# Optimization experiments

Measured on AMD Instinct MI355X. Metric: run time of the kernel, lower is better.

Reference implementation:

```python
import jax, jax.numpy as jnp
import numpy as np

EPS = 1e-5
NUM_GROUPS = 32


def group_norm(x, scale, bias):
    # x: [B, C, H, W], 32 groups, normalized over (C/G, H, W)
    B, C, H, W = x.shape
    G = NUM_GROUPS
    xg = x.reshape(B, G, C // G, H, W)
    mean = xg.mean(axis=(2, 3, 4), keepdims=True)
    var = xg.var(axis=(2, 3, 4), keepdims=True)
    xg = (xg - mean) * jax.lax.rsqrt(var + EPS)
    x = xg.reshape(B, C, H, W)
    return x * scale[None, :, None, None] + bias[None, :, None, None]


def setup_inputs() -> dict:
    key = jax.random.key(0)
    ks = jax.random.split(key, 6)
    B, C, H, W = 32, 512, 32, 32
    std = 1.0 / np.sqrt(C)
    return {
        "x": jax.random.normal(ks[0], (B, C, H, W), dtype=jnp.float32),
        "gn_scale": jnp.ones((C,), dtype=jnp.float32),
        "gn_bias": jnp.zeros((C,), dtype=jnp.float32),
        "wq": jax.random.normal(ks[1], (C, C), dtype=jnp.float32) * std,
        "bq": jnp.zeros((C,), dtype=jnp.float32),
        "wk": jax.random.normal(ks[2], (C, C), dtype=jnp.float32) * std,
        "bk": jnp.zeros((C,), dtype=jnp.float32),
        "wv": jax.random.normal(ks[3], (C, C), dtype=jnp.float32) * std,
        "bv": jnp.zeros((C,), dtype=jnp.float32),
        "wo": jax.random.normal(ks[4], (C, C), dtype=jnp.float32) * std,
        "bo": jnp.zeros((C,), dtype=jnp.float32),
    }


def reference(x, gn_scale, gn_bias, wq, bq, wk, bk, wv, bv, wo, bo):
    B, C, H, W = x.shape
    h = group_norm(x, gn_scale, gn_bias)
    # 1x1 convs == per-pixel matmuls; flatten spatial to tokens: [B, HW, C]
    ht = h.reshape(B, C, H * W).transpose(0, 2, 1)
    q = jnp.einsum('bnc,oc->bno', ht, wq) + bq  # [B, HW, C]
    k = jnp.einsum('bnc,oc->bno', ht, wk) + bk
    v = jnp.einsum('bnc,oc->bno', ht, wv) + bv
    scale = 1.0 / jnp.sqrt(jnp.asarray(C, x.dtype))
    w = jnp.einsum('bnc,bmc->bnm', q, k) * scale  # [B, HW, HW]
    w = jax.nn.softmax(w, axis=-1)
    a = jnp.einsum('bnm,bmc->bnc', w, v)  # [B, HW, C]
    out = jnp.einsum('bnc,oc->bno', a, wo) + bo
    out = out.transpose(0, 2, 1).reshape(B, C, H, W)
    return x + out
```

## Files before the change

### kernel.cpp

```cpp
#include <hip/hip_runtime.h>
#include <stdint.h>

typedef unsigned short u16;
typedef __attribute__((ext_vector_type(8))) short short8;
typedef __attribute__((ext_vector_type(4))) short s16x4;
typedef __attribute__((ext_vector_type(4))) float f32x4;

#define NTOK 1024
#define CDIM 512
#define NG 32

#define GLOAD_LDS16(gptr, lptr)                                                              \
  __builtin_amdgcn_global_load_lds((const __attribute__((address_space(1))) unsigned int*)(gptr), \
                                   (__attribute__((address_space(3))) unsigned int*)(lptr), 16, 0, 0)

__device__ __forceinline__ u16 f2bf(float f) {
  union { float f; uint32_t u; } v; v.f = f;
  uint32_t r = v.u + 0x7fffu + ((v.u >> 16) & 1u);
  return (u16)(r >> 16);
}

__device__ __forceinline__ float bf2f(u16 b) {
  union { uint32_t u; float f; } v; v.u = ((uint32_t)b) << 16;
  return v.f;
}

__global__ __launch_bounds__(256) void wconv(const float* __restrict__ wq, const float* __restrict__ wk,
                                             const float* __restrict__ wv, const float* __restrict__ wo,
                                             const float* __restrict__ bq, const float* __restrict__ bk,
                                             const float* __restrict__ bv,
                                             u16* __restrict__ out, float* __restrict__ bqkv) {
  int i = blockIdx.x * 256 + threadIdx.x;
  out[i]          = f2bf(wq[i]);
  out[262144 + i] = f2bf(wk[i]);
  out[524288 + i] = f2bf(wv[i]);
  out[786432 + i] = f2bf(wo[i]);
  if (i < 512) bqkv[i] = bq[i];
  else if (i < 1024) bqkv[i] = bk[i - 512];
  else if (i < 1536) bqkv[i] = bv[i - 1024];
}

__global__ __launch_bounds__(256) void gn_stats(const float* __restrict__ x,
                                                float* __restrict__ mean_o, float* __restrict__ rstd_o) {
  int bg = blockIdx.x;
  const float4* base = (const float4*)(x + (size_t)bg * 16384);
  float s = 0.f, ss = 0.f;
  for (int i = threadIdx.x; i < 4096; i += 256) {
    float4 v = base[i];
    s  += v.x + v.y + v.z + v.w;
    ss += v.x * v.x + v.y * v.y + v.z * v.z + v.w * v.w;
  }
#pragma unroll
  for (int d = 1; d < 64; d <<= 1) { s += __shfl_xor(s, d); ss += __shfl_xor(ss, d); }
  __shared__ float as[4], as2[4];
  int w = threadIdx.x >> 6;
  if ((threadIdx.x & 63) == 0) { as[w] = s; as2[w] = ss; }
  __syncthreads();
  if (threadIdx.x == 0) {
    float S = as[0] + as[1] + as[2] + as[3];
    float SS = as2[0] + as2[1] + as2[2] + as2[3];
    float m = S * (1.f / 16384.f);
    float var = SS * (1.f / 16384.f) - m * m;
    mean_o[bg] = m;
    rstd_o[bg] = rsqrtf(var + 1e-5f);
  }
}

__global__ __launch_bounds__(256) void gn_apply(const float* __restrict__ x,
                                                const float* __restrict__ mean_, const float* __restrict__ rstd_,
                                                const float* __restrict__ gsc, const float* __restrict__ gbi,
                                                u16* __restrict__ h) {
  int n0 = blockIdx.x * 64, c0 = blockIdx.y * 64, b = blockIdx.z;
  __shared__ u16 t[64][65];
  int tid = threadIdx.x;
  int nl4 = (tid & 15) * 4;
  int clb = tid >> 4;
#pragma unroll
  for (int p = 0; p < 4; ++p) {
    int cl = p * 16 + clb;
    int c = c0 + cl;
    int g = c >> 4;
    float m = mean_[b * NG + g], rs = rstd_[b * NG + g];
    float sc = gsc[c] * rs, bi = gbi[c] - m * sc;
    float4 v = *(const float4*)(x + ((size_t)b * CDIM + c) * NTOK + n0 + nl4);
    t[cl][nl4 + 0] = f2bf(v.x * sc + bi);
    t[cl][nl4 + 1] = f2bf(v.y * sc + bi);
    t[cl][nl4 + 2] = f2bf(v.z * sc + bi);
    t[cl][nl4 + 3] = f2bf(v.w * sc + bi);
  }
  __syncthreads();
  int nl = tid >> 3;
  int cc = (tid & 7) * 8;
#pragma unroll
  for (int p = 0; p < 2; ++p) {
    int n = nl + p * 32;
    short8 o;
#pragma unroll
    for (int i = 0; i < 8; ++i) o[i] = (short)t[cc + i][n];
    *(short8*)(h + (size_t)(b * NTOK + n0 + n) * CDIM + c0 + cc) = o;
  }
}

template <int MODE>
__device__ __forceinline__ void gemm_body(const u16* __restrict__ A, const u16* __restrict__ B,
                                          const float* __restrict__ bias, u16* __restrict__ outb,
                                          u16* __restrict__ outb2,
                                          float* __restrict__ outf, const float* __restrict__ resid,
                                          int Ka, int Kb, int nkt,
                                          size_t strideA, size_t strideB, int batch0) {
  int nx = gridDim.x, ny = gridDim.y;
  int nwg = nx * ny * gridDim.z;
  int id = blockIdx.x + nx * (blockIdx.y + ny * blockIdx.z);
  int cpx = nwg >> 3;
  int sw = (id & 7) * cpx + (id >> 3);
  int bx = sw % nx; int t_ = sw / nx;
  int by = t_ % ny; int z = t_ / ny;

  const u16* Amat = A + (size_t)z * strideA;
  const u16* Bmat = B + (size_t)z * strideB;
  int n0 = bx * 128, m0 = by * 256;
  __shared__ __align__(16) u16 SH[36864];
  int tid = threadIdx.x;
  int l = tid & 63, wid = tid >> 6;
  int lr = l & 15, lh = l >> 4;
  int wm = (wid >> 1) * 64;
  int wn = (wid & 1) * 64;

  f32x4 acc[4][4];
#pragma unroll
  for (int i = 0; i < 4; ++i)
#pragma unroll
    for (int j = 0; j < 4; ++j) acc[i][j] = (f32x4){0.f, 0.f, 0.f, 0.f};

  short8 af[4];
  short8 bfr[4];

  int sr = tid >> 2, sc4 = tid & 3;
  int sg = (sc4 ^ ((sr >> 1) & 3)) * 8;
  const u16* Ag0 = Amat + (size_t)(m0 + sr) * Ka + sg;
  const u16* Ag1 = Ag0 + (size_t)128 * Ka;
  const u16* Bg0 = Bmat + (size_t)(n0 + sr) * Kb + sg;
  u16* Al0 = SH + sr * 32 + sc4 * 8;
  u16* Bl0 = SH + 24576 + sr * 32 + sc4 * 8;

  int rch = (lh ^ ((lr >> 1) & 3)) * 8;

#define STAGE(bufsel, ktv)                                                \
  {                                                                       \
    GLOAD_LDS16(Ag0 + (ktv) * 32, Al0 + (bufsel) * 8192);                 \
    GLOAD_LDS16(Ag1 + (ktv) * 32, Al0 + (bufsel) * 8192 + 4096);          \
    GLOAD_LDS16(Bg0 + (ktv) * 32, Bl0 + (bufsel) * 4096);                 \
  }

#define READ_FRAGS(bufsel)                                                            \
  _Pragma("unroll") for (int i_ = 0; i_ < 4; ++i_)                                    \
    af[i_] = *(const short8*)(SH + (bufsel) * 8192 + (wm + i_ * 16 + lr) * 32 + rch); \
  _Pragma("unroll") for (int j_ = 0; j_ < 4; ++j_)                                    \
    bfr[j_] = *(const short8*)(SH + 24576 + (bufsel) * 4096 + (wn + j_ * 16 + lr) * 32 + rch);

#define MFMA16()                                                                      \
  _Pragma("unroll") for (int i_ = 0; i_ < 4; ++i_)                                    \
    _Pragma("unroll") for (int j_ = 0; j_ < 4; ++j_)                                  \
      acc[i_][j_] = __builtin_amdgcn_mfma_f32_16x16x32_bf16(af[i_], bfr[j_], acc[i_][j_], 0, 0, 0);

  STAGE(0, 0);
  STAGE(1, 1);
  asm volatile("s_waitcnt vmcnt(3)");
  __builtin_amdgcn_sched_barrier(0);
  __builtin_amdgcn_s_barrier();

  int bc = 0, bs = 2;
  for (int t = 0; t < nkt; ++t) {
    const bool more = (t + 2 < nkt);
    if (more) STAGE(bs, t + 2);
    READ_FRAGS(bc);
    __builtin_amdgcn_s_setprio(1);
    MFMA16();
    __builtin_amdgcn_s_setprio(0);
    if (more) { asm volatile("s_waitcnt vmcnt(3)"); }
    else      { asm volatile("s_waitcnt vmcnt(0)"); }
    __builtin_amdgcn_sched_barrier(0);
    __builtin_amdgcn_s_barrier();
    bc = (bc == 2) ? 0 : bc + 1;
    bs = (bs == 2) ? 0 : bs + 1;
  }

  __syncthreads();
  const int gr0 = m0 + wm, gc0 = n0 + wn;
  u16* eb = SH + wid * 4352;

  if constexpr (MODE == 5) {
    float bj[4];
#pragma unroll
    for (int j = 0; j < 4; ++j) bj[j] = bias[gc0 + j * 16 + lr];
    if (n0 < 1024) {
#pragma unroll
      for (int i2 = 0; i2 < 4; ++i2)
#pragma unroll
        for (int j = 0; j < 4; ++j)
#pragma unroll
          for (int r = 0; r < 4; ++r)
            eb[(i2 * 16 + lh * 4 + r) * 68 + j * 16 + lr] = f2bf(acc[i2][j][r] + bj[j]);
      asm volatile("s_waitcnt lgkmcnt(0)");
      __builtin_amdgcn_sched_barrier(0);
#pragma unroll
      for (int t = 0; t < 8; ++t) {
        int row = t * 8 + (l >> 3), c8 = (l & 7) * 8;
        s16x4 lo = *(const s16x4*)(eb + row * 68 + c8);
        s16x4 hi = *(const s16x4*)(eb + row * 68 + c8 + 4);
        short8 o;
        o[0] = lo[0]; o[1] = lo[1]; o[2] = lo[2]; o[3] = lo[3];
        o[4] = hi[0]; o[5] = hi[1]; o[6] = hi[2]; o[7] = hi[3];
        *(short8*)(outb + (size_t)(gr0 + row) * 1024 + gc0 + c8) = o;
      }
    } else {
      int ch0 = gc0 - 1024;
      int bt = m0 >> 10, tok0 = (m0 & 1023) + wm;
#pragma unroll
      for (int i2 = 0; i2 < 4; ++i2)
#pragma unroll
        for (int j = 0; j < 4; ++j) {
          s16x4 w;
#pragma unroll
          for (int r = 0; r < 4; ++r) w[r] = (short)f2bf(acc[i2][j][r] + bj[j]);
          *(s16x4*)(eb + (j * 16 + lr) * 68 + i2 * 16 + lh * 4) = w;
        }
      asm volatile("s_waitcnt lgkmcnt(0)");
      __builtin_amdgcn_sched_barrier(0);
#pragma unroll
      for (int t = 0; t < 8; ++t) {
        int row = t * 8 + (l >> 3), c8 = (l & 7) * 8;
        s16x4 lo = *(const s16x4*)(eb + row * 68 + c8);
        s16x4 hi = *(const s16x4*)(eb + row * 68 + c8 + 4);
        short8 o;
        o[0] = lo[0]; o[1] = lo[1]; o[2] = lo[2]; o[3] = lo[3];
        o[4] = hi[0]; o[5] = hi[1]; o[6] = hi[2]; o[7] = hi[3];
        *(short8*)(outb2 + (size_t)(bt * 512 + ch0 + row) * 1024 + tok0 + c8) = o;
      }
    }
  } else if constexpr (MODE == 3 || MODE == 4) {
    u16* obase = (MODE == 3) ? (outb + (size_t)z * 1048576)
                             : (outb + (size_t)(batch0 + z) * 524288);
    const int LD = (MODE == 3) ? 1024 : 512;
#pragma unroll
    for (int i2 = 0; i2 < 4; ++i2)
#pragma unroll
      for (int j = 0; j < 4; ++j)
#pragma unroll
        for (int r = 0; r < 4; ++r)
          eb[(i2 * 16 + lh * 4 + r) * 68 + j * 16 + lr] = f2bf(acc[i2][j][r]);
    asm volatile("s_waitcnt lgkmcnt(0)");
    __builtin_amdgcn_sched_barrier(0);
#pragma unroll
    for (int t = 0; t < 8; ++t) {
      int row = t * 8 + (l >> 3), c8 = (l & 7) * 8;
      s16x4 lo = *(const s16x4*)(eb + row * 68 + c8);
      s16x4 hi = *(const s16x4*)(eb + row * 68 + c8 + 4);
      short8 o;
      o[0] = lo[0]; o[1] = lo[1]; o[2] = lo[2]; o[3] = lo[3];
      o[4] = hi[0]; o[5] = hi[1]; o[6] = hi[2]; o[7] = hi[3];
      *(short8*)(obase + (size_t)(gr0 + row) * LD + gc0 + c8) = o;
    }
  } else {
    float* ebf = (float*)SH + wid * 2176;
    int bt = n0 >> 10, nn0 = (n0 & 1023) + wn;
#pragma unroll
    for (int pass = 0; pass < 2; ++pass) {
#pragma unroll
      for (int i2 = 0; i2 < 2; ++i2)
#pragma unroll
        for (int r = 0; r < 4; ++r) {
          float bv = bias[gr0 + pass * 32 + i2 * 16 + lh * 4 + r];
#pragma unroll
          for (int j = 0; j < 4; ++j)
            ebf[(i2 * 16 + lh * 4 + r) * 68 + j * 16 + lr] = acc[pass * 2 + i2][j][r] + bv;
        }
      asm volatile("s_waitcnt lgkmcnt(0)");
      __builtin_amdgcn_sched_barrier(0);
#pragma unroll
      for (int t = 0; t < 8; ++t) {
        int row = t * 4 + (l >> 4), c4 = (l & 15) * 4;
        float4 vv = *(const float4*)(ebf + row * 68 + c4);
        size_t addr = ((size_t)bt * 512 + gr0 + pass * 32 + row) * 1024 + nn0 + c4;
        const float4 rr = *(const float4*)(resid + addr);
        vv.x += rr.x; vv.y += rr.y; vv.z += rr.z; vv.w += rr.w;
        *(float4*)(outf + addr) = vv;
      }
      asm volatile("s_waitcnt lgkmcnt(0)");
      __builtin_amdgcn_sched_barrier(0);
    }
  }
#undef STAGE
#undef READ_FRAGS
#undef MFMA16
}

__global__ __launch_bounds__(512, 4) void gemm_qkv(const u16* A, const u16* B, const float* bias,
                                                   u16* outb, u16* outb2, float* outf, const float* resid,
                                                   int Ka, int Kb, int nkt, size_t sA, size_t sB, int b0) {
  gemm_body<5>(A, B, bias, outb, outb2, outf, resid, Ka, Kb, nkt, sA, sB, b0);
}
__global__ __launch_bounds__(512, 4) void gemm_o(const u16* A, const u16* B, const float* bias,
                                                 u16* outb, u16* outb2, float* outf, const float* resid,
                                                 int Ka, int Kb, int nkt, size_t sA, size_t sB, int b0) {
  gemm_body<2>(A, B, bias, outb, outb2, outf, resid, Ka, Kb, nkt, sA, sB, b0);
}
__global__ __launch_bounds__(512, 4) void gemm_s(const u16* A, const u16* B, const float* bias,
                                                 u16* outb, u16* outb2, float* outf, const float* resid,
                                                 int Ka, int Kb, int nkt, size_t sA, size_t sB, int b0) {
  gemm_body<3>(A, B, bias, outb, outb2, outf, resid, Ka, Kb, nkt, sA, sB, b0);
}
__global__ __launch_bounds__(512, 4) void gemm_pv(const u16* A, const u16* B, const float* bias,
                                                  u16* outb, u16* outb2, float* outf, const float* resid,
                                                  int Ka, int Kb, int nkt, size_t sA, size_t sB, int b0) {
  gemm_body<4>(A, B, bias, outb, outb2, outf, resid, Ka, Kb, nkt, sA, sB, b0);
}

__global__ __launch_bounds__(256) void softmax_rows(u16* __restrict__ S) {
  const float scale = 0.04419417382415922f;
  int row = blockIdx.x * 4 + (threadIdx.x >> 6);
  int l = threadIdx.x & 63;
  u16* Sr = S + (size_t)row * 1024;
  short8 a = *(const short8*)(Sr + l * 8);
  short8 b = *(const short8*)(Sr + 512 + l * 8);
  float f[16];
#pragma unroll
  for (int i = 0; i < 8; ++i) { f[i] = bf2f((u16)a[i]); f[8 + i] = bf2f((u16)b[i]); }
  float mx = f[0];
#pragma unroll
  for (int i = 1; i < 16; ++i) mx = fmaxf(mx, f[i]);
#pragma unroll
  for (int d = 1; d < 64; d <<= 1) mx = fmaxf(mx, __shfl_xor(mx, d));
  float s = 0.f;
#pragma unroll
  for (int i = 0; i < 16; ++i) { f[i] = __expf((f[i] - mx) * scale); s += f[i]; }
#pragma unroll
  for (int d = 1; d < 64; d <<= 1) s += __shfl_xor(s, d);
  float inv = 1.f / s;
  short8 oa, ob;
#pragma unroll
  for (int i = 0; i < 8; ++i) { oa[i] = (short)f2bf(f[i] * inv); ob[i] = (short)f2bf(f[8 + i] * inv); }
  *(short8*)(Sr + l * 8) = oa;
  *(short8*)(Sr + 512 + l * 8) = ob;
}

extern "C" void kernel_launch(void* const* d_in, const int* in_sizes, int n_in,
                              void* d_out, int out_size, void* d_ws, size_t ws_size,
                              hipStream_t stream) {
  const float* x   = (const float*)d_in[0];
  const float* gsc = (const float*)d_in[1];
  const float* gbi = (const float*)d_in[2];
  const float* wq  = (const float*)d_in[3];
  const float* bq  = (const float*)d_in[4];
  const float* wk  = (const float*)d_in[5];
  const float* bk  = (const float*)d_in[6];
  const float* wv  = (const float*)d_in[7];
  const float* bv  = (const float*)d_in[8];
  const float* wo  = (const float*)d_in[9];
  const float* bo  = (const float*)d_in[10];

  char* ws = (char*)d_ws;
  u16* wbf = (u16*)ws;
  float* bqkv = (float*)(ws + (2ull << 20));
  float* mean_ = (float*)(ws + (2ull << 20) + 65536);
  float* rstd_ = mean_ + 1024;
  u16* h   = (u16*)(ws + (4ull << 20));
  u16* qk  = (u16*)(ws + (36ull << 20));
  u16* vm  = (u16*)(ws + (100ull << 20));
  u16* S   = (u16*)(ws + (132ull << 20));
  u16* am  = h;
  float* out = (float*)d_out;

  size_t sbytes = ws_size > (132ull << 20) ? ws_size - (132ull << 20) : 0;
  int CB = 1;
  while (CB < 32 && (size_t)(CB * 2) * (2ull << 20) <= sbytes) CB *= 2;

  wconv<<<1024, 256, 0, stream>>>(wq, wk, wv, wo, bq, bk, bv, wbf, bqkv);
  gn_stats<<<1024, 256, 0, stream>>>(x, mean_, rstd_);
  gn_apply<<<dim3(16, 8, 32), 256, 0, stream>>>(x, mean_, rstd_, gsc, gbi, h);
  gemm_qkv<<<dim3(12, 128), 512, 0, stream>>>(h, wbf, bqkv, qk, vm, nullptr, nullptr,
                                              512, 512, 16, 0, 0, 0);
  for (int c0 = 0; c0 < 32; c0 += CB) {
    gemm_s<<<dim3(8, 4, CB), 512, 0, stream>>>(qk + (size_t)c0 * 1048576, qk + 512 + (size_t)c0 * 1048576,
                                               nullptr, S, nullptr, nullptr, nullptr,
                                               1024, 1024, 16, 1048576, 1048576, 0);
    softmax_rows<<<CB * 256, 256, 0, stream>>>(S);
    gemm_pv<<<dim3(4, 4, CB), 512, 0, stream>>>(S, vm + (size_t)c0 * 524288,
                                                nullptr, am, nullptr, nullptr, nullptr,
                                                1024, 1024, 32, 1048576, 524288, c0);
  }
  gemm_o<<<dim3(256, 2), 512, 0, stream>>>(wbf + 786432, am, bo, nullptr, nullptr, out, x,
                                           512, 512, 16, 0, 0, 0);
}
```

Measured before the change: 248.3 us.

## Halve GEMM workgroup to four waves with 128x64 per-wave tiles

All four GEMM kernels now run 256 threads (4 waves) per 256x128 block instead of 8 waves. Each wave computes a 128x64 output tile with 8x4 MFMA accumulators, and the staging issues six global-to-LDS loads per thread per k-step. Epilogues are split into two passes so the per-wave LDS scratch still fits. The larger per-wave tile raises register reuse of fragments, but accumulator register pressure roughly doubles and occupancy drops (launch bounds 256,2), which can expose memory latency.

Measured after the change: 248.2 us. No clear change (-0.0%).

```diff
diff --git a/kernel.cpp b/kernel.cpp
--- a/kernel.cpp
+++ b/kernel.cpp
@@ -123,49 +123,51 @@
   int tid = threadIdx.x;
   int l = tid & 63, wid = tid >> 6;
   int lr = l & 15, lh = l >> 4;
-  int wm = (wid >> 1) * 64;
+  int wm = (wid >> 1) * 128;
   int wn = (wid & 1) * 64;
 
-  f32x4 acc[4][4];
-#pragma unroll
-  for (int i = 0; i < 4; ++i)
+  f32x4 acc[8][4];
+#pragma unroll
+  for (int i = 0; i < 8; ++i)
 #pragma unroll
     for (int j = 0; j < 4; ++j) acc[i][j] = (f32x4){0.f, 0.f, 0.f, 0.f};
 
-  short8 af[4];
+  short8 af[8];
   short8 bfr[4];
 
   int sr = tid >> 2, sc4 = tid & 3;
   int sg = (sc4 ^ ((sr >> 1) & 3)) * 8;
   const u16* Ag0 = Amat + (size_t)(m0 + sr) * Ka + sg;
-  const u16* Ag1 = Ag0 + (size_t)128 * Ka;
   const u16* Bg0 = Bmat + (size_t)(n0 + sr) * Kb + sg;
   u16* Al0 = SH + sr * 32 + sc4 * 8;
   u16* Bl0 = SH + 24576 + sr * 32 + sc4 * 8;
 
   int rch = (lh ^ ((lr >> 1) & 3)) * 8;
 
-#define STAGE(bufsel, ktv)                                                \
-  {                                                                       \
-    GLOAD_LDS16(Ag0 + (ktv) * 32, Al0 + (bufsel) * 8192);                 \
-    GLOAD_LDS16(Ag1 + (ktv) * 32, Al0 + (bufsel) * 8192 + 4096);          \
-    GLOAD_LDS16(Bg0 + (ktv) * 32, Bl0 + (bufsel) * 4096);                 \
+#define STAGE(bufsel, ktv)                                                        \
+  {                                                                               \
+    GLOAD_LDS16(Ag0 + (ktv) * 32,                       Al0 + (bufsel) * 8192);   \
+    GLOAD_LDS16(Ag0 + (ktv) * 32 + (size_t)64  * Ka,    Al0 + (bufsel) * 8192 + 2048); \
+    GLOAD_LDS16(Ag0 + (ktv) * 32 + (size_t)128 * Ka,    Al0 + (bufsel) * 8192 + 4096); \
+    GLOAD_LDS16(Ag0 + (ktv) * 32 + (size_t)192 * Ka,    Al0 + (bufsel) * 8192 + 6144); \
+    GLOAD_LDS16(Bg0 + (ktv) * 32,                       Bl0 + (bufsel) * 4096);   \
+    GLOAD_LDS16(Bg0 + (ktv) * 32 + (size_t)64  * Kb,    Bl0 + (bufsel) * 4096 + 2048); \
   }
 
 #define READ_FRAGS(bufsel)                                                            \
-  _Pragma("unroll") for (int i_ = 0; i_ < 4; ++i_)                                    \
+  _Pragma("unroll") for (int i_ = 0; i_ < 8; ++i_)                                    \
     af[i_] = *(const short8*)(SH + (bufsel) * 8192 + (wm + i_ * 16 + lr) * 32 + rch); \
   _Pragma("unroll") for (int j_ = 0; j_ < 4; ++j_)                                    \
     bfr[j_] = *(const short8*)(SH + 24576 + (bufsel) * 4096 + (wn + j_ * 16 + lr) * 32 + rch);
 
-#define MFMA16()                                                                      \
-  _Pragma("unroll") for (int i_ = 0; i_ < 4; ++i_)                                    \
+#define MFMA32()                                                                      \
+  _Pragma("unroll") for (int i_ = 0; i_ < 8; ++i_)                                    \
     _Pragma("unroll") for (int j_ = 0; j_ < 4; ++j_)                                  \
       acc[i_][j_] = __builtin_amdgcn_mfma_f32_16x16x32_bf16(af[i_], bfr[j_], acc[i_][j_], 0, 0, 0);
 
   STAGE(0, 0);
   STAGE(1, 1);
-  asm volatile("s_waitcnt vmcnt(3)");
+  asm volatile("s_waitcnt vmcnt(6)");
   __builtin_amdgcn_sched_barrier(0);
   __builtin_amdgcn_s_barrier();
 
@@ -175,9 +177,9 @@
     if (more) STAGE(bs, t + 2);
     READ_FRAGS(bc);
     __builtin_amdgcn_s_setprio(1);
-    MFMA16();
+    MFMA32();
     __builtin_amdgcn_s_setprio(0);
-    if (more) { asm volatile("s_waitcnt vmcnt(3)"); }
+    if (more) { asm volatile("s_waitcnt vmcnt(6)"); }
     else      { asm volatile("s_waitcnt vmcnt(0)"); }
     __builtin_amdgcn_sched_barrier(0);
     __builtin_amdgcn_s_barrier();
@@ -195,12 +197,73 @@
     for (int j = 0; j < 4; ++j) bj[j] = bias[gc0 + j * 16 + lr];
     if (n0 < 1024) {
 #pragma unroll
+      for (int pass = 0; pass < 2; ++pass) {
+#pragma unroll
+        for (int i2 = 0; i2 < 4; ++i2)
+#pragma unroll
+          for (int j = 0; j < 4; ++j)
+#pragma unroll
+            for (int r = 0; r < 4; ++r)
+              eb[(i2 * 16 + lh * 4 + r) * 68 + j * 16 + lr] =
+                  f2bf(acc[pass * 4 + i2][j][r] + bj[j]);
+        asm volatile("s_waitcnt lgkmcnt(0)");
+        __builtin_amdgcn_sched_barrier(0);
+#pragma unroll
+        for (int t = 0; t < 8; ++t) {
+          int row = t * 8 + (l >> 3), c8 = (l & 7) * 8;
+          s16x4 lo = *(const s16x4*)(eb + row * 68 + c8);
+          s16x4 hi = *(const s16x4*)(eb + row * 68 + c8 + 4);
+          short8 o;
+          o[0] = lo[0]; o[1] = lo[1]; o[2] = lo[2]; o[3] = lo[3];
+          o[4] = hi[0]; o[5] = hi[1]; o[6] = hi[2]; o[7] = hi[3];
+          *(short8*)(outb + (size_t)(gr0 + pass * 64 + row) * 1024 + gc0 + c8) = o;
+        }
+        asm volatile("s_waitcnt lgkmcnt(0)");
+        __builtin_amdgcn_sched_barrier(0);
+      }
+    } else {
+      int ch0 = gc0 - 1024;
+      int bt = m0 >> 10, tok0 = (m0 & 1023) + wm;
+#pragma unroll
+      for (int pass = 0; pass < 2; ++pass) {
+#pragma unroll
+        for (int i2 = 0; i2 < 4; ++i2)
+#pragma unroll
+          for (int j = 0; j < 4; ++j) {
+            s16x4 w;
+#pragma unroll
+            for (int r = 0; r < 4; ++r) w[r] = (short)f2bf(acc[pass * 4 + i2][j][r] + bj[j]);
+            *(s16x4*)(eb + (j * 16 + lr) * 68 + i2 * 16 + lh * 4) = w;
+          }
+        asm volatile("s_waitcnt lgkmcnt(0)");
+        __builtin_amdgcn_sched_barrier(0);
+#pragma unroll
+        for (int t = 0; t < 8; ++t) {
+          int row = t * 8 + (l >> 3), c8 = (l & 7) * 8;
+          s16x4 lo = *(const s16x4*)(eb + row * 68 + c8);
+          s16x4 hi = *(const s16x4*)(eb + row * 68 + c8 + 4);
+          short8 o;
+          o[0] = lo[0]; o[1] = lo[1]; o[2] = lo[2]; o[3] = lo[3];
+          o[4] = hi[0]; o[5] = hi[1]; o[6] = hi[2]; o[7] = hi[3];
+          *(short8*)(outb2 + (size_t)(bt * 512 + ch0 + row) * 1024 + tok0 + pass * 64 + c8) = o;
+        }
+        asm volatile("s_waitcnt lgkmcnt(0)");
+        __builtin_amdgcn_sched_barrier(0);
+      }
+    }
+  } else if constexpr (MODE == 3 || MODE == 4) {
+    u16* obase = (MODE == 3) ? (outb + (size_t)z * 1048576)
+                             : (outb + (size_t)(batch0 + z) * 524288);
+    const int LD = (MODE == 3) ? 1024 : 512;
+#pragma unroll
+    for (int pass = 0; pass < 2; ++pass) {
+#pragma unroll
       for (int i2 = 0; i2 < 4; ++i2)
 #pragma unroll
         for (int j = 0; j < 4; ++j)
 #pragma unroll
           for (int r = 0; r < 4; ++r)
-            eb[(i2 * 16 + lh * 4 + r) * 68 + j * 16 + lr] = f2bf(acc[i2][j][r] + bj[j]);
+            eb[(i2 * 16 + lh * 4 + r) * 68 + j * 16 + lr] = f2bf(acc[pass * 4 + i2][j][r]);
       asm volatile("s_waitcnt lgkmcnt(0)");
       __builtin_amdgcn_sched_barrier(0);
 #pragma unroll
@@ -211,61 +274,16 @@
         short8 o;
         o[0] = lo[0]; o[1] = lo[1]; o[2] = lo[2]; o[3] = lo[3];
         o[4] = hi[0]; o[5] = hi[1]; o[6] = hi[2]; o[7] = hi[3];
-        *(short8*)(outb + (size_t)(gr0 + row) * 1024 + gc0 + c8) = o;
+        *(short8*)(obase + (size_t)(gr0 + pass * 64 + row) * LD + gc0 + c8) = o;
       }
-    } else {
-      int ch0 = gc0 - 1024;
-      int bt = m0 >> 10, tok0 = (m0 & 1023) + wm;
-#pragma unroll
-      for (int i2 = 0; i2 < 4; ++i2)
-#pragma unroll
-        for (int j = 0; j < 4; ++j) {
-          s16x4 w;
-#pragma unroll
-          for (int r = 0; r < 4; ++r) w[r] = (short)f2bf(acc[i2][j][r] + bj[j]);
-          *(s16x4*)(eb + (j * 16 + lr) * 68 + i2 * 16 + lh * 4) = w;
-        }
       asm volatile("s_waitcnt lgkmcnt(0)");
       __builtin_amdgcn_sched_barrier(0);
-#pragma unroll
-      for (int t = 0; t < 8; ++t) {
-        int row = t * 8 + (l >> 3), c8 = (l & 7) * 8;
-        s16x4 lo = *(const s16x4*)(eb + row * 68 + c8);
-        s16x4 hi = *(const s16x4*)(eb + row * 68 + c8 + 4);
-        short8 o;
-        o[0] = lo[0]; o[1] = lo[1]; o[2] = lo[2]; o[3] = lo[3];
-        o[4] = hi[0]; o[5] = hi[1]; o[6] = hi[2]; o[7] = hi[3];
-        *(short8*)(outb2 + (size_t)(bt * 512 + ch0 + row) * 1024 + tok0 + c8) = o;
-      }
-    }
-  } else if constexpr (MODE == 3 || MODE == 4) {
-    u16* obase = (MODE == 3) ? (outb + (size_t)z * 1048576)
-                             : (outb + (size_t)(batch0 + z) * 524288);
-    const int LD = (MODE == 3) ? 1024 : 512;
-#pragma unroll
-    for (int i2 = 0; i2 < 4; ++i2)
-#pragma unroll
-      for (int j = 0; j < 4; ++j)
-#pragma unroll
-        for (int r = 0; r < 4; ++r)
-          eb[(i2 * 16 + lh * 4 + r) * 68 + j * 16 + lr] = f2bf(acc[i2][j][r]);
-    asm volatile("s_waitcnt lgkmcnt(0)");
-    __builtin_amdgcn_sched_barrier(0);
-#pragma unroll
-    for (int t = 0; t < 8; ++t) {
-      int row = t * 8 + (l >> 3), c8 = (l & 7) * 8;
-      s16x4 lo = *(const s16x4*)(eb + row * 68 + c8);
-      s16x4 hi = *(const s16x4*)(eb + row * 68 + c8 + 4);
-      short8 o;
-      o[0] = lo[0]; o[1] = lo[1]; o[2] = lo[2]; o[3] = lo[3];
-      o[4] = hi[0]; o[5] = hi[1]; o[6] = hi[2]; o[7] = hi[3];
-      *(short8*)(obase + (size_t)(gr0 + row) * LD + gc0 + c8) = o;
     }
   } else {
     float* ebf = (float*)SH + wid * 2176;
     int bt = n0 >> 10, nn0 = (n0 & 1023) + wn;
 #pragma unroll
-    for (int pass = 0; pass < 2; ++pass) {
+    for (int pass = 0; pass < 4; ++pass) {
 #pragma unroll
       for (int i2 = 0; i2 < 2; ++i2)
 #pragma unroll
@@ -292,25 +310,25 @@
   }
 #undef STAGE
 #undef READ_FRAGS
-#undef MFMA16
-}
-
-__global__ __launch_bounds__(512, 4) void gemm_qkv(const u16* A, const u16* B, const float* bias,
+#undef MFMA32
+}
+
+__global__ __launch_bounds__(256, 2) void gemm_qkv(const u16* A, const u16* B, const float* bias,
                                                    u16* outb, u16* outb2, float* outf, const float* resid,
                                                    int Ka, int Kb, int nkt, size_t sA, size_t sB, int b0) {
   gemm_body<5>(A, B, bias, outb, outb2, outf, resid, Ka, Kb, nkt, sA, sB, b0);
 }
-__global__ __launch_bounds__(512, 4) void gemm_o(const u16* A, const u16* B, const float* bias,
+__global__ __launch_bounds__(256, 2) void gemm_o(const u16* A, const u16* B, const float* bias,
                                                  u16* outb, u16* outb2, float* outf, const float* resid,
                                                  int Ka, int Kb, int nkt, size_t sA, size_t sB, int b0) {
   gemm_body<2>(A, B, bias, outb, outb2, outf, resid, Ka, Kb, nkt, sA, sB, b0);
 }
-__global__ __launch_bounds__(512, 4) void gemm_s(const u16* A, const u16* B, const float* bias,
+__global__ __launch_bounds__(256, 2) void gemm_s(const u16* A, const u16* B, const float* bias,
                                                  u16* outb, u16* outb2, float* outf, const float* resid,
                                                  int Ka, int Kb, int nkt, size_t sA, size_t sB, int b0) {
   gemm_body<3>(A, B, bias, outb, outb2, outf, resid, Ka, Kb, nkt, sA, sB, b0);
 }
-__global__ __launch_bounds__(512, 4) void gemm_pv(const u16* A, const u16* B, const float* bias,
+__global__ __launch_bounds__(256, 2) void gemm_pv(const u16* A, const u16* B, const float* bias,
                                                   u16* outb, u16* outb2, float* outf, const float* resid,
                                                   int Ka, int Kb, int nkt, size_t sA, size_t sB, int b0) {
   gemm_body<4>(A, B, bias, outb, outb2, outf, resid, Ka, Kb, nkt, sA, sB, b0);
@@ -378,17 +396,17 @@
   wconv<<<1024, 256, 0, stream>>>(wq, wk, wv, wo, bq, bk, bv, wbf, bqkv);
   gn_stats<<<1024, 256, 0, stream>>>(x, mean_, rstd_);
   gn_apply<<<dim3(16, 8, 32), 256, 0, stream>>>(x, mean_, rstd_, gsc, gbi, h);
-  gemm_qkv<<<dim3(12, 128), 512, 0, stream>>>(h, wbf, bqkv, qk, vm, nullptr, nullptr,
+  gemm_qkv<<<dim3(12, 128), 256, 0, stream>>>(h, wbf, bqkv, qk, vm, nullptr, nullptr,
                                               512, 512, 16, 0, 0, 0);
   for (int c0 = 0; c0 < 32; c0 += CB) {
-    gemm_s<<<dim3(8, 4, CB), 512, 0, stream>>>(qk + (size_t)c0 * 1048576, qk + 512 + (size_t)c0 * 1048576,
+    gemm_s<<<dim3(8, 4, CB), 256, 0, stream>>>(qk + (size_t)c0 * 1048576, qk + 512 + (size_t)c0 * 1048576,
                                                nullptr, S, nullptr, nullptr, nullptr,
                                                1024, 1024, 16, 1048576, 1048576, 0);
     softmax_rows<<<CB * 256, 256, 0, stream>>>(S);
-    gemm_pv<<<dim3(4, 4, CB), 512, 0, stream>>>(S, vm + (size_t)c0 * 524288,
+    gemm_pv<<<dim3(4, 4, CB), 256, 0, stream>>>(S, vm + (size_t)c0 * 524288,
                                                 nullptr, am, nullptr, nullptr, nullptr,
                                                 1024, 1024, 32, 1048576, 524288, c0);
   }
-  gemm_o<<<dim3(256, 2), 512, 0, stream>>>(wbf + 786432, am, bo, nullptr, nullptr, out, x,
+  gemm_o<<<dim3(256, 2), 256, 0, stream>>>(wbf + 786432, am, bo, nullptr, nullptr, out, x,
                                            512, 512, 16, 0, 0, 0);
 }
```
